# Kernel optimization log

Measured on AMD Instinct MI355X. Metric: run time of the kernel, lower is better.

The kernel has to match this reference:

```python
import jax, jax.numpy as jnp
import numpy as np

EPS = 1e-5
SLOPE = 0.2
K = 20
BINS = [1, 2, 4, 8, 16, 32]


def knn(x_t, k):
    # x_t: (B, N, C) -> idx (B, N, k) of nearest neighbors (by L2, incl. self)
    xx = jnp.sum(x_t * x_t, axis=-1)  # (B, N)
    pd = 2.0 * jnp.einsum('bnc,bmc->bnm', x_t, x_t) - xx[:, :, None] - xx[:, None, :]
    _, idx = jax.lax.top_k(pd, k)
    return idx


def edge_features(x_t, idx):
    # x_t: (B, N, C), idx: (B, N, k) -> (B, N, k, 2C) = [nbr - ctr, ctr]
    B = x_t.shape[0]
    nbr = x_t[jnp.arange(B)[:, None, None], idx]          # (B, N, k, C) gather
    ctr = jnp.broadcast_to(x_t[:, :, None, :], nbr.shape)
    return jnp.concatenate([nbr - ctr, ctr], axis=-1)


def batchnorm(h, gamma, beta, axes):
    # training-mode BN: normalize with batch statistics over `axes` (channel last)
    m = jnp.mean(h, axis=axes, keepdims=True)
    v = jnp.var(h, axis=axes, keepdims=True)
    return (h - m) * jax.lax.rsqrt(v + EPS) * gamma + beta


def lrelu(h):
    return jnp.where(h >= 0, h, SLOPE * h)


def edgeconv(x_t, W, g, b):
    # 1x1 conv over edge features + BN + LeakyReLU + max over k neighbors
    e = edge_features(x_t, knn(x_t, K))            # (B, N, k, 2C)
    h = jnp.einsum('bnkc,oc->bnko', e, W)          # per-edge GEMM
    h = lrelu(batchnorm(h, g, b, (0, 1, 2)))
    return jnp.max(h, axis=2)                      # (B, N, Cout)


def setup_inputs() -> dict:
    key = jax.random.key(0)
    ks = jax.random.split(key, 8)
    B, N = 4, 2048
    d = {'x': jax.random.normal(ks[0], (B, 3, N), dtype=jnp.float32)}
    # conv weights (out, in); BN gamma=1, beta=0 as in torch init
    d['W1'] = jax.random.normal(ks[1], (64, 6), dtype=jnp.float32) * 0.1
    d['g1'] = jnp.ones((64,), jnp.float32); d['b1'] = jnp.zeros((64,), jnp.float32)
    d['W2'] = jax.random.normal(ks[2], (64, 128), dtype=jnp.float32) * 0.1
    d['g2'] = jnp.ones((64,), jnp.float32); d['b2'] = jnp.zeros((64,), jnp.float32)
    d['W3'] = jax.random.normal(ks[3], (128, 128), dtype=jnp.float32) * 0.1
    d['g3'] = jnp.ones((128,), jnp.float32); d['b3'] = jnp.zeros((128,), jnp.float32)
    d['W4'] = jax.random.normal(ks[4], (256, 256), dtype=jnp.float32) * 0.1
    d['g4'] = jnp.ones((256,), jnp.float32); d['b4'] = jnp.zeros((256,), jnp.float32)
    d['W5'] = jax.random.normal(ks[5], (1024, 512), dtype=jnp.float32) * 0.05
    d['g5'] = jnp.ones((1024,), jnp.float32); d['b5'] = jnp.zeros((1024,), jnp.float32)
    d['Wf'] = jax.random.normal(ks[6], (256, 1024), dtype=jnp.float32) * 0.03
    d['bfeat'] = jax.random.normal(ks[7], (256,), dtype=jnp.float32) * 0.01
    return d


def reference(x, W1, g1, b1, W2, g2, b2, W3, g3, b3, W4, g4, b4, W5, g5, b5, Wf, bfeat):
    B, _, N = x.shape
    x_t = jnp.transpose(x, (0, 2, 1))              # (B, N, 3)
    x1 = edgeconv(x_t, W1, g1, b1)                 # (B, N, 64)
    x2 = edgeconv(x1, W2, g2, b2)                  # (B, N, 64)
    x3 = edgeconv(x2, W3, g3, b3)                  # (B, N, 128)
    x4 = edgeconv(x3, W4, g4, b4)                  # (B, N, 256)
    xc = jnp.concatenate([x1, x2, x3, x4], axis=-1)  # (B, N, 512)
    h = jnp.einsum('bnc,oc->bno', xc, W5)          # (B, N, 1024)
    h = lrelu(batchnorm(h, g5, b5, (0, 1)))
    F = h.shape[-1]
    feats = []
    for nb in BINS:  # horizontal pyramid pooling over contiguous point chunks
        z = h.reshape(B, nb, N // nb, F)
        feats.append(jnp.max(z, axis=2) + jnp.mean(z, axis=2))
    bins = jnp.concatenate(feats, axis=1)          # (B, 63, F)
    out = jnp.einsum('bsf,of->sbo', bins, Wf) + bfeat  # (63, B, 256)
    return out
```

## Files before the change

### kernel.cpp

```cpp
#include <hip/hip_runtime.h>
#include <hip/hip_bf16.h>
#include <cstdint>
#include <cstddef>

#define B_SZ   4
#define N_PTS  2048
#define KNN    20
#define BN_ROWS (B_SZ * N_PTS)
#define EPSV   1e-5f
#define SLOPEV 0.2f

typedef __attribute__((ext_vector_type(8))) short bf16x8;
typedef __attribute__((ext_vector_type(4))) float f32x4;

__global__ void k_transpose(const float* __restrict__ x, float* __restrict__ xt,
                            float* __restrict__ xx)
{
    int i = blockIdx.x * 256 + threadIdx.x;
    if (i >= BN_ROWS) return;
    int b = i >> 11, n = i & 2047;
    float v0 = x[((b * 3 + 0) << 11) + n];
    float v1 = x[((b * 3 + 1) << 11) + n];
    float v2 = x[((b * 3 + 2) << 11) + n];
    xt[i * 3 + 0] = v0; xt[i * 3 + 1] = v1; xt[i * 3 + 2] = v2;
    xx[i] = fmaf(v0, v0, fmaf(v1, v1, v2 * v2));
}

__global__ void k_prepw_all(const float* __restrict__ W1, const float* __restrict__ W2,
                            const float* __restrict__ W3, const float* __restrict__ W4,
                            const float* __restrict__ W5, const float* __restrict__ Wf,
                            float* __restrict__ wc, __hip_bfloat16* __restrict__ w5h,
                            float* __restrict__ wft)
{
    int i = blockIdx.x * 256 + threadIdx.x;
    if (i >= 876928) return;
    if (i >= 614784) {
        int e = i - 614784;
        int o = e >> 10, f = e & 1023;
        wft[f * 256 + o] = Wf[e];
        return;
    }
    if (i >= 90496) {
        int e = i - 90496;
        w5h[e] = __float2bfloat16(W5[e]);
        return;
    }
    const float* W; int O, C, off;
    if      (i < 384)   { W = W1; O = 64;  C = 3;   off = 0; }
    else if (i < 8576)  { W = W2; O = 64;  C = 64;  off = 384; }
    else if (i < 24960) { W = W3; O = 128; C = 64;  off = 8576; }
    else                { W = W4; O = 256; C = 128; off = 24960; }
    int e = i - off, j = e / C, c = e - j * C;
    float v;
    if (j < O) v = W[j * 2 * C + c];
    else { int jo = j - O; v = W[jo * 2 * C + C + c] - W[jo * 2 * C + c]; }
    wc[i] = v;
}

template<bool VEC>
__launch_bounds__(512)
__global__ void k_dist(const float* __restrict__ A, int lda,
                       const float* __restrict__ xx,
                       float* __restrict__ C1, int Kd)
{
    constexpr int LDA_ = 132;
    constexpr int LDT_ = 68;
    __shared__ float smem[8704];
    float* As = smem;
    float* Bs = smem + 32 * LDA_;
    float* T  = smem;
    const int tid = threadIdx.x;
    const int tx  = tid & 31;
    const int ty  = tid >> 5;

    int t = blockIdx.x;
    int it, jt;
    if (t < 120) {
        int i = 0;
        for (; i < 15; ++i) { int cnt = 15 - i; if (t < cnt) break; t -= cnt; }
        it = i; jt = i + 1 + t;
    } else {
        it = jt = t - 120;
    }
    const int m0 = it * 128;
    const int n0 = jt * 128;
    const int b  = blockIdx.z;
    const float* Ab = A + (size_t)b * N_PTS * lda;

    float acc[2][4][4] = {};

    for (int k0 = 0; k0 < Kd; k0 += 32) {
        #pragma unroll
        for (int r = 0; r < 2; ++r) {
            int e = r * 512 + tid, row = e >> 3, kq = e & 7;
            if constexpr (VEC) {
                float4 v = *(const float4*)&Ab[(size_t)(m0 + row) * lda + k0 + kq * 4];
                As[(kq * 4 + 0) * LDA_ + row] = v.x;
                As[(kq * 4 + 1) * LDA_ + row] = v.y;
                As[(kq * 4 + 2) * LDA_ + row] = v.z;
                As[(kq * 4 + 3) * LDA_ + row] = v.w;
            } else {
                #pragma unroll
                for (int j = 0; j < 4; ++j) {
                    int kg = k0 + kq * 4 + j;
                    As[(kq * 4 + j) * LDA_ + row] =
                        (kg < Kd) ? Ab[(size_t)(m0 + row) * lda + kg] : 0.f;
                }
            }
        }
        #pragma unroll
        for (int r = 0; r < 2; ++r) {
            int e = r * 512 + tid, row = e >> 3, kq = e & 7;
            if constexpr (VEC) {
                float4 v = *(const float4*)&Ab[(size_t)(n0 + row) * lda + k0 + kq * 4];
                Bs[(kq * 4 + 0) * LDA_ + row] = v.x;
                Bs[(kq * 4 + 1) * LDA_ + row] = v.y;
                Bs[(kq * 4 + 2) * LDA_ + row] = v.z;
                Bs[(kq * 4 + 3) * LDA_ + row] = v.w;
            } else {
                #pragma unroll
                for (int j = 0; j < 4; ++j) {
                    int kg = k0 + kq * 4 + j;
                    Bs[(kq * 4 + j) * LDA_ + row] =
                        (kg < Kd) ? Ab[(size_t)(n0 + row) * lda + kg] : 0.f;
                }
            }
        }
        __syncthreads();

        if constexpr (VEC) {
            float4 ca0 = *(const float4*)&As[ty * 4];
            float4 ca1 = *(const float4*)&As[64 + ty * 4];
            float4 cb  = *(const float4*)&Bs[tx * 4];
            #pragma unroll
            for (int kk = 0; kk < 32; ++kk) {
                float4 na0, na1, nb;
                if (kk < 31) {
                    na0 = *(const float4*)&As[(kk + 1) * LDA_ + ty * 4];
                    na1 = *(const float4*)&As[(kk + 1) * LDA_ + 64 + ty * 4];
                    nb  = *(const float4*)&Bs[(kk + 1) * LDA_ + tx * 4];
                }
                float av[2][4] = {{ca0.x,ca0.y,ca0.z,ca0.w},{ca1.x,ca1.y,ca1.z,ca1.w}};
                float bw[4] = {cb.x, cb.y, cb.z, cb.w};
                #pragma unroll
                for (int ih = 0; ih < 2; ++ih)
                    #pragma unroll
                    for (int ii = 0; ii < 4; ++ii)
                        #pragma unroll
                        for (int jj = 0; jj < 4; ++jj)
                            acc[ih][ii][jj] = fmaf(av[ih][ii], bw[jj], acc[ih][ii][jj]);
                if (kk < 31) { ca0 = na0; ca1 = na1; cb = nb; }
            }
        } else {
            int klen = Kd - k0; if (klen > 32) klen = 32;
            #pragma unroll 8
            for (int kk = 0; kk < klen; ++kk) {
                float4 a0 = *(const float4*)&As[kk * LDA_ + ty * 4];
                float4 a1 = *(const float4*)&As[kk * LDA_ + 64 + ty * 4];
                float4 bq = *(const float4*)&Bs[kk * LDA_ + tx * 4];
                float av[2][4] = {{a0.x,a0.y,a0.z,a0.w},{a1.x,a1.y,a1.z,a1.w}};
                float bw[4] = {bq.x, bq.y, bq.z, bq.w};
                #pragma unroll
                for (int ih = 0; ih < 2; ++ih)
                    #pragma unroll
                    for (int ii = 0; ii < 4; ++ii)
                        #pragma unroll
                        for (int jj = 0; jj < 4; ++jj)
                            acc[ih][ii][jj] = fmaf(av[ih][ii], bw[jj], acc[ih][ii][jj]);
            }
        }
        __syncthreads();
    }

    const float* xxb = xx + b * N_PTS;
    float xj[4];
    {
        float4 v = *(const float4*)&xxb[n0 + tx * 4];
        xj[0] = v.x; xj[1] = v.y; xj[2] = v.z; xj[3] = v.w;
    }
    float xiv[2][4];
    #pragma unroll
    for (int ih = 0; ih < 2; ++ih)
        #pragma unroll
        for (int i = 0; i < 4; ++i)
            xiv[ih][i] = xxb[m0 + ih * 64 + ty * 4 + i];
    const bool diag = (m0 == n0);
    const size_t zoff = (size_t)b * N_PTS;

    #pragma unroll
    for (int ih = 0; ih < 2; ++ih)
        #pragma unroll
        for (int i = 0; i < 4; ++i) {
            int gi = m0 + ih * 64 + ty * 4 + i;
            float xi = xiv[ih][i];
            int gj = n0 + tx * 4;
            float4 v;
            v.x = 2.f * acc[ih][i][0] - xi - xj[0];
            v.y = 2.f * acc[ih][i][1] - xi - xj[1];
            v.z = 2.f * acc[ih][i][2] - xi - xj[2];
            v.w = 2.f * acc[ih][i][3] - xi - xj[3];
            if (diag) {
                if (gi == gj + 0) v.x = 0.f;
                if (gi == gj + 1) v.y = 0.f;
                if (gi == gj + 2) v.z = 0.f;
                if (gi == gj + 3) v.w = 0.f;
            }
            *(float4*)&C1[(zoff + gi) * N_PTS + gj] = v;
        }

    if (!diag) {
        #pragma unroll
        for (int ih = 0; ih < 2; ++ih) {
            #pragma unroll
            for (int c = 0; c < 4; ++c) {
                float xjc = xj[c];
                float4 tv;
                tv.x = 2.f * acc[ih][0][c] - xjc - xiv[ih][0];
                tv.y = 2.f * acc[ih][1][c] - xjc - xiv[ih][1];
                tv.z = 2.f * acc[ih][2][c] - xjc - xiv[ih][2];
                tv.w = 2.f * acc[ih][3][c] - xjc - xiv[ih][3];
                *(float4*)&T[(tx * 4 + c) * LDT_ + ty * 4] = tv;
            }
            __syncthreads();
            #pragma unroll
            for (int r = 0; r < 4; ++r) {
                int e = r * 512 + tid;
                int jr = e >> 4, c4 = e & 15;
                float4 tv = *(const float4*)&T[jr * LDT_ + c4 * 4];
                *(float4*)&C1[(zoff + n0 + jr) * N_PTS + m0 + ih * 64 + c4 * 4] = tv;
            }
            __syncthreads();
        }
    }
}

__launch_bounds__(256)
__global__ void k_gemm5(const unsigned short* __restrict__ Ah,
                        const unsigned short* __restrict__ Bh,
                        float* __restrict__ Cf,
                        float* __restrict__ ssum, float* __restrict__ ssumsq)
{
    constexpr int LDA = 72;
    __shared__ unsigned short As[128 * LDA];
    __shared__ unsigned short Bs[128 * LDA];
    const int tid  = threadIdx.x;
    const int lane = tid & 63;
    const int w    = tid >> 6;
    const int wr   = w >> 1, wcl = w & 1;
    const int quad = lane >> 4;
    const int l16  = lane & 15;
    const int m0 = blockIdx.y * 128;
    const int n0 = blockIdx.x * 128;

    f32x4 acc[4][4] = {};

    for (int k0 = 0; k0 < 512; k0 += 64) {
        #pragma unroll
        for (int r = 0; r < 4; ++r) {
            int e = r * 256 + tid, row = e >> 3, kq = e & 7;
            *(uint4*)&As[row * LDA + kq * 8] =
                *(const uint4*)&Ah[(size_t)(m0 + row) * 512 + k0 + kq * 8];
        }
        #pragma unroll
        for (int r = 0; r < 4; ++r) {
            int e = r * 256 + tid, row = e >> 3, kq = e & 7;
            *(uint4*)&Bs[row * LDA + kq * 8] =
                *(const uint4*)&Bh[(size_t)(n0 + row) * 512 + k0 + kq * 8];
        }
        __syncthreads();
        #pragma unroll
        for (int kk = 0; kk < 64; kk += 32) {
            bf16x8 af[4], bfr[4];
            #pragma unroll
            for (int i = 0; i < 4; ++i)
                af[i] = *(const bf16x8*)&As[(wr * 64 + i * 16 + l16) * LDA + kk + quad * 8];
            #pragma unroll
            for (int j = 0; j < 4; ++j)
                bfr[j] = *(const bf16x8*)&Bs[(wcl * 64 + j * 16 + l16) * LDA + kk + quad * 8];
            #pragma unroll
            for (int i = 0; i < 4; ++i)
                #pragma unroll
                for (int j = 0; j < 4; ++j)
                    acc[i][j] = __builtin_amdgcn_mfma_f32_16x16x32_bf16(af[i], bfr[j], acc[i][j], 0, 0, 0);
        }
        __syncthreads();
    }

    #pragma unroll
    for (int i = 0; i < 4; ++i) {
        int rbase = m0 + wr * 64 + i * 16 + quad * 4;
        #pragma unroll
        for (int j = 0; j < 4; ++j) {
            int col = n0 + wcl * 64 + j * 16 + l16;
            #pragma unroll
            for (int r = 0; r < 4; ++r)
                Cf[(size_t)(rbase + r) * 1024 + col] = acc[i][j][r];
        }
    }

    float* sredS = (float*)As;
    float* sredQ = (float*)Bs;
    #pragma unroll
    for (int j = 0; j < 4; ++j) {
        float s = 0.f, q = 0.f;
        #pragma unroll
        for (int i = 0; i < 4; ++i)
            #pragma unroll
            for (int r = 0; r < 4; ++r) {
                float v = acc[i][j][r];
                s += v; q = fmaf(v, v, q);
            }
        int coll = wcl * 64 + j * 16 + l16;
        int slot = wr * 4 + quad;
        sredS[coll * 8 + slot] = s;
        sredQ[coll * 8 + slot] = q;
    }
    __syncthreads();
    if (tid < 128) {
        float s = 0.f, q = 0.f;
        #pragma unroll
        for (int t = 0; t < 8; ++t) { s += sredS[tid * 8 + t]; q += sredQ[tid * 8 + t]; }
        ssum  [blockIdx.y * 1024 + n0 + tid] = s;
        ssumsq[blockIdx.y * 1024 + n0 + tid] = q;
    }
}

template<bool VEC>
__launch_bounds__(256)
__global__ void k_selgd(const float* __restrict__ D2, int* __restrict__ idx_out,
                        const float* __restrict__ A, int lda,
                        const float* __restrict__ Bm, int ldb,
                        float* __restrict__ C1, float* __restrict__ C2,
                        int Nn, int Kd, int gdBlocks, int gdsh)
{
    constexpr int LDA_ = 132;
    constexpr int LDB_ = 68;
    __shared__ float smem[32 * LDA_ + 32 * LDB_];

    if ((int)blockIdx.x < gdBlocks) {
        float* As = smem;
        float* Bs = smem + 32 * LDA_;
        const int tid = threadIdx.x;
        const int tx  = tid & 15;
        const int ty  = tid >> 4;
        const int gdx = Nn >> 6;
        const int bx  = blockIdx.x & (gdx - 1);
        const int by  = blockIdx.x >> gdsh;
        const int m0 = by * 128;
        const int n0 = bx * 64;

        float acc[2][4][4] = {};

        for (int k0 = 0; k0 < Kd; k0 += 32) {
            #pragma unroll
            for (int r = 0; r < 4; ++r) {
                int e = r * 256 + tid, row = e >> 3, kq = e & 7;
                if constexpr (VEC) {
                    float4 v = *(const float4*)&A[(size_t)(m0 + row) * lda + k0 + kq * 4];
                    As[(kq * 4 + 0) * LDA_ + row] = v.x;
                    As[(kq * 4 + 1) * LDA_ + row] = v.y;
                    As[(kq * 4 + 2) * LDA_ + row] = v.z;
                    As[(kq * 4 + 3) * LDA_ + row] = v.w;
                } else {
                    #pragma unroll
                    for (int j = 0; j < 4; ++j) {
                        int kg = k0 + kq * 4 + j;
                        As[(kq * 4 + j) * LDA_ + row] =
                            (kg < Kd) ? A[(size_t)(m0 + row) * lda + kg] : 0.f;
                    }
                }
            }
            #pragma unroll
            for (int r = 0; r < 2; ++r) {
                int e = r * 256 + tid, row = e >> 3, kq = e & 7;
                if constexpr (VEC) {
                    float4 v = *(const float4*)&Bm[(size_t)(n0 + row) * ldb + k0 + kq * 4];
                    Bs[(kq * 4 + 0) * LDB_ + row] = v.x;
                    Bs[(kq * 4 + 1) * LDB_ + row] = v.y;
                    Bs[(kq * 4 + 2) * LDB_ + row] = v.z;
                    Bs[(kq * 4 + 3) * LDB_ + row] = v.w;
                } else {
                    #pragma unroll
                    for (int j = 0; j < 4; ++j) {
                        int kg = k0 + kq * 4 + j;
                        Bs[(kq * 4 + j) * LDB_ + row] =
                            (kg < Kd) ? Bm[(size_t)(n0 + row) * ldb + kg] : 0.f;
                    }
                }
            }
            __syncthreads();

            if constexpr (VEC) {
                float4 ca0 = *(const float4*)&As[ty * 4];
                float4 ca1 = *(const float4*)&As[64 + ty * 4];
                float4 cb0 = *(const float4*)&Bs[tx * 4];
                #pragma unroll
                for (int kk = 0; kk < 32; ++kk) {
                    float4 na0, na1, nb0;
                    if (kk < 31) {
                        na0 = *(const float4*)&As[(kk + 1) * LDA_ + ty * 4];
                        na1 = *(const float4*)&As[(kk + 1) * LDA_ + 64 + ty * 4];
                        nb0 = *(const float4*)&Bs[(kk + 1) * LDB_ + tx * 4];
                    }
                    float av[2][4] = {{ca0.x,ca0.y,ca0.z,ca0.w},{ca1.x,ca1.y,ca1.z,ca1.w}};
                    float bw[4] = {cb0.x, cb0.y, cb0.z, cb0.w};
                    #pragma unroll
                    for (int ih = 0; ih < 2; ++ih)
                        #pragma unroll
                        for (int ii = 0; ii < 4; ++ii)
                            #pragma unroll
                            for (int jj = 0; jj < 4; ++jj)
                                acc[ih][ii][jj] = fmaf(av[ih][ii], bw[jj], acc[ih][ii][jj]);
                    if (kk < 31) { ca0 = na0; ca1 = na1; cb0 = nb0; }
                }
            } else {
                int klen = Kd - k0; if (klen > 32) klen = 32;
                #pragma unroll 8
                for (int kk = 0; kk < klen; ++kk) {
                    float4 a0 = *(const float4*)&As[kk * LDA_ + ty * 4];
                    float4 a1 = *(const float4*)&As[kk * LDA_ + 64 + ty * 4];
                    float4 bq = *(const float4*)&Bs[kk * LDB_ + tx * 4];
                    float av[2][4] = {{a0.x,a0.y,a0.z,a0.w},{a1.x,a1.y,a1.z,a1.w}};
                    float bw[4] = {bq.x, bq.y, bq.z, bq.w};
                    #pragma unroll
                    for (int ih = 0; ih < 2; ++ih)
                        #pragma unroll
                        for (int ii = 0; ii < 4; ++ii)
                            #pragma unroll
                            for (int jj = 0; jj < 4; ++jj)
                                acc[ih][ii][jj] = fmaf(av[ih][ii], bw[jj], acc[ih][ii][jj]);
                }
            }
            __syncthreads();
        }

        const int Oo = Nn >> 1;
        #pragma unroll
        for (int ih = 0; ih < 2; ++ih)
            #pragma unroll
            for (int i = 0; i < 4; ++i) {
                int row = m0 + ih * 64 + ty * 4 + i;
                int colg = n0 + tx * 4;
                float4 v = make_float4(acc[ih][i][0], acc[ih][i][1],
                                       acc[ih][i][2], acc[ih][i][3]);
                if (colg < Oo) *(float4*)&C1[(size_t)row * Oo + colg] = v;
                else           *(float4*)&C2[(size_t)row * Oo + colg - Oo] = v;
            }
        return;
    }

    const int lane = threadIdx.x & 63;
    const int w    = threadIdx.x >> 6;
    const int qloc = ((int)blockIdx.x - gdBlocks) * 4 + w;
    const float* row = D2 + (size_t)qloc * N_PTS;

    unsigned key[32];
    #pragma unroll
    for (int c = 0; c < 8; ++c) {
        float4 v = *(const float4*)&row[c * 256 + lane * 4];
        float vv[4] = {v.x, v.y, v.z, v.w};
        #pragma unroll
        for (int r = 0; r < 4; ++r) {
            unsigned u = __float_as_uint(vv[r]);
            key[c * 4 + r] = ((int)u >= 0) ? (u | 0x80000000u) : ~u;
        }
    }

    unsigned lmax = 0u;
    #pragma unroll
    for (int e = 0; e < 32; ++e) lmax = (key[e] > lmax) ? key[e] : lmax;
    unsigned gmin = lmax, gmax = lmax;
    #pragma unroll
    for (int s = 32; s >= 1; s >>= 1) {
        unsigned o1 = __shfl_xor(gmin, s, 64);
        unsigned o2 = __shfl_xor(gmax, s, 64);
        gmin = (o1 < gmin) ? o1 : gmin;
        gmax = (o2 > gmax) ? o2 : gmax;
    }
    unsigned lo = gmin, hi = gmax;

    while (hi - lo >= 65536u) {
        unsigned mid = lo + ((hi - lo) >> 1);
        int cnt = 0;
        #pragma unroll
        for (int e = 0; e < 32; ++e)
            cnt += __popcll(__ballot(key[e] > mid));
        if (cnt < KNN) hi = mid; else lo = mid + 1;
    }

    if (lo < hi) {
        int cAbove = 0;
        #pragma unroll
        for (int e = 0; e < 32; ++e)
            cAbove += __popcll(__ballot(key[e] > hi));
        unsigned c0 = 0u, c1 = 0u, c2 = 0u, c3 = 0u;
        int nc = 0;
        #pragma unroll
        for (int e = 0; e < 32; ++e) {
            unsigned k = key[e];
            if (k >= lo && k <= hi) {
                if (nc == 0) c0 = k; else if (nc == 1) c1 = k;
                else if (nc == 2) c2 = k; else if (nc == 3) c3 = k;
                ++nc;
            }
        }
        if (__ballot(nc > 4)) {
            while (lo < hi) {
                unsigned mid = lo + ((hi - lo) >> 1);
                int cnt = 0;
                #pragma unroll
                for (int e = 0; e < 32; ++e)
                    cnt += __popcll(__ballot(key[e] > mid));
                if (cnt < KNN) hi = mid; else lo = mid + 1;
            }
        } else {
            while (lo < hi) {
                unsigned mid = lo + ((hi - lo) >> 1);
                int cnt = cAbove
                        + __popcll(__ballot(c0 > mid))
                        + __popcll(__ballot(c1 > mid))
                        + __popcll(__ballot(c2 > mid))
                        + __popcll(__ballot(c3 > mid));
                if (cnt < KNN) hi = mid; else lo = mid + 1;
            }
        }
    }
    const unsigned T = lo;

    int* outp = idx_out + (size_t)qloc * KNN;
    const unsigned long long ltmask = (lane == 0) ? 0ull : (~0ull >> (64 - lane));
    int base = 0;
    #pragma unroll
    for (int e = 0; e < 32; ++e) {
        bool p = key[e] > T;
        unsigned long long m = __ballot(p);
        if (p) {
            int pos = base + __popcll(m & ltmask);
            outp[pos] = (e >> 2) * 256 + lane * 4 + (e & 3);
        }
        base += __popcll(m);
    }
    #pragma unroll
    for (int e = 0; e < 32; ++e) {
        bool p = key[e] == T;
        unsigned long long m = __ballot(p);
        if (p) {
            int pos = base + __popcll(m & ltmask);
            if (pos < KNN) outp[pos] = (e >> 2) * 256 + lane * 4 + (e & 3);
        }
        base += __popcll(m);
    }
}

template<int O, int NSEQ>
__launch_bounds__(256)
__global__ void k_gather(const float* __restrict__ gtab, const float* __restrict__ dtab,
                         const int* __restrict__ idx,
                         float* __restrict__ hmax, float* __restrict__ hmin,
                         float* __restrict__ ssum, float* __restrict__ ssumsq)
{
    constexpr int NPB = 256 / O;
    const int grp = threadIdx.x / O;
    const int o   = threadIdx.x & (O - 1);
    float accS = 0.f, accS2 = 0.f;
    const int rowsPerBlock = NPB * NSEQ;
    const int batch = blockIdx.x & 3;
    const int chunk = blockIdx.x >> 2;
    const int bbase = batch << 11;
    for (int s = 0; s < NSEQ; ++s) {
        int row = bbase + chunk * rowsPerBlock + s * NPB + grp;
        const int* ip = idx + (size_t)row * KNN;
        float gmax = -INFINITY, gmin = INFINITY, gs = 0.f, gs2 = 0.f;
        for (int k = 0; k < KNN; ++k) {
            int nb = ip[k];
            float v = gtab[(size_t)(bbase + nb) * O + o];
            gmax = fmaxf(gmax, v);
            gmin = fminf(gmin, v);
            gs  += v;
            gs2  = fmaf(v, v, gs2);
        }
        float d = dtab[(size_t)row * O + o];
        hmax[(size_t)row * O + o] = gmax + d;
        hmin[(size_t)row * O + o] = gmin + d;
        accS  += gs + (float)KNN * d;
        accS2 += gs2 + 2.f * d * gs + (float)KNN * d * d;
    }
    int bank = blockIdx.x & 63;
    atomicAdd(&ssum[bank * O + o], accS);
    atomicAdd(&ssumsq[bank * O + o], accS2);
}

template<int O, bool WRITE_XX>
__launch_bounds__(256)
__global__ void k_normalize(const float* __restrict__ hmax, const float* __restrict__ hmin,
                            const float* __restrict__ ssum, const float* __restrict__ ssumsq,
                            const float* __restrict__ gamma, const float* __restrict__ beta,
                            float invM, float* __restrict__ xcs,
                            __hip_bfloat16* __restrict__ xch, float* __restrict__ xx)
{
    const int tid = threadIdx.x;
    const int o   = tid & (O - 1);
    float s = 0.f, s2 = 0.f;
    #pragma unroll 8
    for (int bk = 0; bk < 64; ++bk) { s += ssum[bk * O + o]; s2 += ssumsq[bk * O + o]; }
    float mean = s * invM;
    float var  = fmaf(-mean, mean, s2 * invM);
    float sc   = gamma[o] * rsqrtf(var + EPSV);
    float sh   = beta[o] - mean * sc;

    constexpr int R = 256 / O;
    const int rloc = tid / O;
    __shared__ float part[4];
    const int ngroups = BN_ROWS / R;
    for (int gidx = blockIdx.x; gidx < ngroups; gidx += gridDim.x) {
        int row = gidx * R + rloc;
        size_t i = (size_t)row * O + o;
        float h = (sc >= 0.f) ? hmax[i] : hmin[i];
        float y = fmaf(h, sc, sh);
        y = (y >= 0.f) ? y : SLOPEV * y;
        xcs[(size_t)row * 512 + o] = y;
        xch[(size_t)row * 512 + o] = __float2bfloat16(y);
        if constexpr (WRITE_XX) {
            float p = y * y;
            #pragma unroll
            for (int sft = 32; sft >= 1; sft >>= 1) p += __shfl_xor(p, sft, 64);
            if constexpr (O == 64) {
                if ((tid & 63) == 0) xx[row] = p;
            } else {
                if ((tid & 63) == 0) part[tid >> 6] = p;
                __syncthreads();
                if constexpr (O == 128) {
                    if (tid < 2) xx[gidx * R + tid] = part[2 * tid] + part[2 * tid + 1];
                } else {
                    if (tid == 0) xx[gidx * R] = (part[0] + part[1]) + (part[2] + part[3]);
                }
                __syncthreads();
            }
        }
    }
}

__global__ void k_seg(const float* __restrict__ h,
                      const float* __restrict__ ssum, const float* __restrict__ ssumsq,
                      const float* __restrict__ gamma, const float* __restrict__ beta,
                      float* __restrict__ smax, float* __restrict__ ssumseg)
{
    int f = blockIdx.y * 256 + threadIdx.x;
    float s = 0.f, s2 = 0.f;
    #pragma unroll 8
    for (int bk = 0; bk < 64; ++bk) { s += ssum[bk * 1024 + f]; s2 += ssumsq[bk * 1024 + f]; }
    const float invM = 1.f / (float)BN_ROWS;
    float mean = s * invM;
    float var  = fmaf(-mean, mean, s2 * invM);
    float sc   = gamma[f] * rsqrtf(var + EPSV);
    float sh   = beta[f] - mean * sc;

    int seg = blockIdx.x;
    float mx = -INFINITY, sm = 0.f;
    int n0 = seg * 64;
    for (int i = 0; i < 64; ++i) {
        float v = fmaf(h[(size_t)(n0 + i) * 1024 + f], sc, sh);
        v = (v >= 0.f) ? v : SLOPEV * v;
        mx = fmaxf(mx, v); sm += v;
    }
    smax[(size_t)seg * 1024 + f]    = mx;
    ssumseg[(size_t)seg * 1024 + f] = sm;
}

__launch_bounds__(256)
__global__ void k_final(const float* __restrict__ smax, const float* __restrict__ ssg,
                        const float* __restrict__ Wft, const float* __restrict__ bfeat,
                        float* __restrict__ out)
{
    __shared__ float row[1024];
    __shared__ float part[1024];
    const int tid = threadIdx.x;
    int sb = blockIdx.x;
    int s = sb >> 2, b = sb & 3;
    int nb = (s == 0) ? 1 : (s < 3) ? 2 : (s < 7) ? 4 : (s < 15) ? 8 : (s < 31) ? 16 : 32;
    int idxL = s - (nb - 1);
    int segc = 32 / nb;
    int seg0 = b * 32 + idxL * segc;
    float inv = 1.f / (float)(64 * segc);
    for (int c = tid; c < 1024; c += 256) {
        float mx = -INFINITY, sm = 0.f;
        for (int t = 0; t < segc; ++t) {
            mx = fmaxf(mx, smax[(size_t)(seg0 + t) * 1024 + c]);
            sm += ssg[(size_t)(seg0 + t) * 1024 + c];
        }
        row[c] = mx + sm * inv;
    }
    __syncthreads();

    const int lane = tid & 63;
    const int w    = tid >> 6;
    const float* rw = row + w * 256;
    const float* wp = Wft + (size_t)(w * 256) * 256 + lane * 4;
    float4 a0 = {0,0,0,0}, a1 = {0,0,0,0}, a2 = {0,0,0,0}, a3 = {0,0,0,0};
    for (int f = 0; f < 256; f += 4) {
        float r0 = rw[f + 0], r1 = rw[f + 1], r2 = rw[f + 2], r3 = rw[f + 3];
        float4 w0 = *(const float4*)&wp[(size_t)(f + 0) * 256];
        float4 w1 = *(const float4*)&wp[(size_t)(f + 1) * 256];
        float4 w2 = *(const float4*)&wp[(size_t)(f + 2) * 256];
        float4 w3 = *(const float4*)&wp[(size_t)(f + 3) * 256];
        a0.x = fmaf(r0, w0.x, a0.x); a0.y = fmaf(r0, w0.y, a0.y);
        a0.z = fmaf(r0, w0.z, a0.z); a0.w = fmaf(r0, w0.w, a0.w);
        a1.x = fmaf(r1, w1.x, a1.x); a1.y = fmaf(r1, w1.y, a1.y);
        a1.z = fmaf(r1, w1.z, a1.z); a1.w = fmaf(r1, w1.w, a1.w);
        a2.x = fmaf(r2, w2.x, a2.x); a2.y = fmaf(r2, w2.y, a2.y);
        a2.z = fmaf(r2, w2.z, a2.z); a2.w = fmaf(r2, w2.w, a2.w);
        a3.x = fmaf(r3, w3.x, a3.x); a3.y = fmaf(r3, w3.y, a3.y);
        a3.z = fmaf(r3, w3.z, a3.z); a3.w = fmaf(r3, w3.w, a3.w);
    }
    float4 a;
    a.x = (a0.x + a1.x) + (a2.x + a3.x);
    a.y = (a0.y + a1.y) + (a2.y + a3.y);
    a.z = (a0.z + a1.z) + (a2.z + a3.z);
    a.w = (a0.w + a1.w) + (a2.w + a3.w);
    *(float4*)&part[w * 256 + lane * 4] = a;
    __syncthreads();
    int o = tid;
    float acc = (part[o] + part[256 + o]) + (part[512 + o] + part[768 + o]);
    out[(size_t)sb * 256 + o] = acc + bfeat[o];
}

extern "C" void kernel_launch(void* const* d_in, const int* in_sizes, int n_in,
                              void* d_out, int out_size, void* d_ws, size_t ws_size,
                              hipStream_t stream)
{
    const float* x  = (const float*)d_in[0];
    const float* W1 = (const float*)d_in[1];
    const float* g1 = (const float*)d_in[2];
    const float* b1 = (const float*)d_in[3];
    const float* W2 = (const float*)d_in[4];
    const float* g2 = (const float*)d_in[5];
    const float* b2 = (const float*)d_in[6];
    const float* W3 = (const float*)d_in[7];
    const float* g3 = (const float*)d_in[8];
    const float* b3 = (const float*)d_in[9];
    const float* W4 = (const float*)d_in[10];
    const float* g4 = (const float*)d_in[11];
    const float* b4 = (const float*)d_in[12];
    const float* W5 = (const float*)d_in[13];
    const float* g5 = (const float*)d_in[14];
    const float* b5 = (const float*)d_in[15];
    const float* Wf = (const float*)d_in[16];
    const float* bfeat = (const float*)d_in[17];
    float* out = (float*)d_out;
    float* ws  = (float*)d_ws;

    float* xt1   = ws + 0;
    int*   idx   = (int*)(ws + 24576);
    float* xx    = ws + 188416;
    float* xc    = ws + 196608;
    float* hmax  = ws + 4390912;
    float* hmin  = ws + 6488064;
    float* stats = ws + 8585216;
    float* smax  = ws + 8650752;
    float* ssg   = ws + 8781824;
    float* wc    = ws + 8912896;
    float* big   = ws + 9003520;
    __hip_bfloat16* xch = (__hip_bfloat16*)(ws + 25780736);
    __hip_bfloat16* w5h = (__hip_bfloat16*)(ws + 27877888);
    float* wft   = ws + 28140032;
    float* l5s   = ws + 28402176;
    float* l5q   = ws + 28467712;
    float* gtab  = ws + 28533248;
    float* dtab  = ws + 30630400;

    hipMemsetAsync(stats, 0, 65536 * sizeof(float), stream);
    k_transpose<<<32, 256, 0, stream>>>(x, xt1, xx);
    k_prepw_all<<<3426, 256, 0, stream>>>(W1, W2, W3, W4, W5, Wf, wc, w5h, wft);

    const float invMk = 1.f / (float)(BN_ROWS * KNN);

    {
        float* ss = stats + 0;
        k_dist<false><<<dim3(136, 1, 4), 512, 0, stream>>>(xt1, 3, xx, big, 3);
        k_selgd<false><<<128 + 2048, 256, 0, stream>>>(big, idx, xt1, 3, wc, 3, gtab, dtab, 128, 3, 128, 1);
        k_gather<64, 8><<<256, 256, 0, stream>>>(gtab, dtab, idx, hmax, hmin, ss, ss + 4096);
        k_normalize<64, true><<<512, 256, 0, stream>>>(hmax, hmin, ss, ss + 4096, g1, b1, invMk, xc + 0, xch + 0, xx);
    }
    {
        float* ss = stats + 8192;
        k_dist<true><<<dim3(136, 1, 4), 512, 0, stream>>>(xc + 0, 512, xx, big, 64);
        k_selgd<true><<<128 + 2048, 256, 0, stream>>>(big, idx, xc + 0, 512, wc + 384, 64, gtab, dtab, 128, 64, 128, 1);
        k_gather<64, 8><<<256, 256, 0, stream>>>(gtab, dtab, idx, hmax, hmin, ss, ss + 4096);
        k_normalize<64, true><<<512, 256, 0, stream>>>(hmax, hmin, ss, ss + 4096, g2, b2, invMk, xc + 64, xch + 64, xx);
    }
    {
        float* ss = stats + 16384;
        k_dist<true><<<dim3(136, 1, 4), 512, 0, stream>>>(xc + 64, 512, xx, big, 64);
        k_selgd<true><<<256 + 2048, 256, 0, stream>>>(big, idx, xc + 64, 512, wc + 8576, 64, gtab, dtab, 256, 64, 256, 2);
        k_gather<128, 8><<<512, 256, 0, stream>>>(gtab, dtab, idx, hmax, hmin, ss, ss + 8192);
        k_normalize<128, true><<<512, 256, 0, stream>>>(hmax, hmin, ss, ss + 8192, g3, b3, invMk, xc + 128, xch + 128, xx);
    }
    {
        float* ss = stats + 32768;
        k_dist<true><<<dim3(136, 1, 4), 512, 0, stream>>>(xc + 128, 512, xx, big, 128);
        k_selgd<true><<<512 + 2048, 256, 0, stream>>>(big, idx, xc + 128, 512, wc + 24960, 128, gtab, dtab, 512, 128, 512, 3);
        k_gather<256, 8><<<1024, 256, 0, stream>>>(gtab, dtab, idx, hmax, hmin, ss, ss + 16384);
        k_normalize<256, false><<<512, 256, 0, stream>>>(hmax, hmin, ss, ss + 16384, g4, b4, invMk, xc + 256, xch + 256, xx);
    }
    {
        k_gemm5<<<dim3(8, 64), 256, 0, stream>>>((const unsigned short*)xch, (const unsigned short*)w5h, big, l5s, l5q);
        k_seg<<<dim3(128, 4), 256, 0, stream>>>(big, l5s, l5q, g5, b5, smax, ssg);
        k_final<<<252, 256, 0, stream>>>(smax, ssg, wft, bfeat, out);
    }
}
```

Before: 490.3 us.

## Pre-select max/min by gamma sign in gather and rework top-k threshold search

The gather kernel now writes a single buffer holding either the per-channel max or min, chosen by the sign of gamma (since sc = gamma*rsqrt(var+eps) has gamma's sign). This halves the gather kernel's writes and the normalize kernel's reads. The selection kernel's threshold search now first binary-searches on per-lane maxima, then collects candidates at or above that bound, falling back to a full-key search if any lane has more than four. This is meant to cut ballot iterations, but it may cost extra iterations when many lanes overflow.

Result: no change. 488.2 us (median of 3 runs) (-0.4%).

```diff
diff --git a/kernel.cpp b/kernel.cpp
--- a/kernel.cpp
+++ b/kernel.cpp
@@ -477,52 +477,43 @@
         gmin = (o1 < gmin) ? o1 : gmin;
         gmax = (o2 > gmax) ? o2 : gmax;
     }
-    unsigned lo = gmin, hi = gmax;
-
-    while (hi - lo >= 65536u) {
-        unsigned mid = lo + ((hi - lo) >> 1);
-        int cnt = 0;
-        #pragma unroll
-        for (int e = 0; e < 32; ++e)
-            cnt += __popcll(__ballot(key[e] > mid));
-        if (cnt < KNN) hi = mid; else lo = mid + 1;
-    }
-
-    if (lo < hi) {
-        int cAbove = 0;
-        #pragma unroll
-        for (int e = 0; e < 32; ++e)
-            cAbove += __popcll(__ballot(key[e] > hi));
-        unsigned c0 = 0u, c1 = 0u, c2 = 0u, c3 = 0u;
-        int nc = 0;
-        #pragma unroll
-        for (int e = 0; e < 32; ++e) {
-            unsigned k = key[e];
-            if (k >= lo && k <= hi) {
-                if (nc == 0) c0 = k; else if (nc == 1) c1 = k;
-                else if (nc == 2) c2 = k; else if (nc == 3) c3 = k;
-                ++nc;
-            }
-        }
-        if (__ballot(nc > 4)) {
-            while (lo < hi) {
-                unsigned mid = lo + ((hi - lo) >> 1);
-                int cnt = 0;
-                #pragma unroll
-                for (int e = 0; e < 32; ++e)
-                    cnt += __popcll(__ballot(key[e] > mid));
-                if (cnt < KNN) hi = mid; else lo = mid + 1;
-            }
-        } else {
-            while (lo < hi) {
-                unsigned mid = lo + ((hi - lo) >> 1);
-                int cnt = cAbove
-                        + __popcll(__ballot(c0 > mid))
-                        + __popcll(__ballot(c1 > mid))
-                        + __popcll(__ballot(c2 > mid))
-                        + __popcll(__ballot(c3 > mid));
-                if (cnt < KNN) hi = mid; else lo = mid + 1;
-            }
+
+    unsigned lo = gmin, hi2 = gmax;
+    while (lo < hi2) {
+        unsigned mid = lo + ((hi2 - lo) >> 1);
+        int c = __popcll(__ballot(lmax > mid));
+        if (c < KNN) hi2 = mid; else lo = mid + 1;
+    }
+    unsigned hi = gmax;
+
+    unsigned c0 = 0u, c1 = 0u, c2 = 0u, c3 = 0u;
+    int nc = 0;
+    #pragma unroll
+    for (int e = 0; e < 32; ++e) {
+        unsigned k = key[e];
+        if (k >= lo) {
+            if (nc == 0) c0 = k; else if (nc == 1) c1 = k;
+            else if (nc == 2) c2 = k; else if (nc == 3) c3 = k;
+            ++nc;
+        }
+    }
+    if (__ballot(nc > 4)) {
+        while (lo < hi) {
+            unsigned mid = lo + ((hi - lo) >> 1);
+            int cnt = 0;
+            #pragma unroll
+            for (int e = 0; e < 32; ++e)
+                cnt += __popcll(__ballot(key[e] > mid));
+            if (cnt < KNN) hi = mid; else lo = mid + 1;
+        }
+    } else {
+        while (lo < hi) {
+            unsigned mid = lo + ((hi - lo) >> 1);
+            int cnt = __popcll(__ballot(c0 > mid))
+                    + __popcll(__ballot(c1 > mid))
+                    + __popcll(__ballot(c2 > mid))
+                    + __popcll(__ballot(c3 > mid));
+            if (cnt < KNN) hi = mid; else lo = mid + 1;
         }
     }
     const unsigned T = lo;
@@ -555,13 +546,14 @@
 template<int O, int NSEQ>
 __launch_bounds__(256)
 __global__ void k_gather(const float* __restrict__ gtab, const float* __restrict__ dtab,
-                         const int* __restrict__ idx,
-                         float* __restrict__ hmax, float* __restrict__ hmin,
+                         const int* __restrict__ idx, const float* __restrict__ gamma,
+                         float* __restrict__ hsel,
                          float* __restrict__ ssum, float* __restrict__ ssumsq)
 {
     constexpr int NPB = 256 / O;
     const int grp = threadIdx.x / O;
     const int o   = threadIdx.x & (O - 1);
+    const float g = gamma[o];
     float accS = 0.f, accS2 = 0.f;
     const int rowsPerBlock = NPB * NSEQ;
     const int batch = blockIdx.x & 3;
@@ -580,8 +572,8 @@
             gs2  = fmaf(v, v, gs2);
         }
         float d = dtab[(size_t)row * O + o];
-        hmax[(size_t)row * O + o] = gmax + d;
-        hmin[(size_t)row * O + o] = gmin + d;
+        float keep = (g >= 0.f) ? gmax : gmin;
+        hsel[(size_t)row * O + o] = keep + d;
         accS  += gs + (float)KNN * d;
         accS2 += gs2 + 2.f * d * gs + (float)KNN * d * d;
     }
@@ -592,7 +584,7 @@
 
 template<int O, bool WRITE_XX>
 __launch_bounds__(256)
-__global__ void k_normalize(const float* __restrict__ hmax, const float* __restrict__ hmin,
+__global__ void k_normalize(const float* __restrict__ hsel,
                             const float* __restrict__ ssum, const float* __restrict__ ssumsq,
                             const float* __restrict__ gamma, const float* __restrict__ beta,
                             float invM, float* __restrict__ xcs,
@@ -615,7 +607,7 @@
     for (int gidx = blockIdx.x; gidx < ngroups; gidx += gridDim.x) {
         int row = gidx * R + rloc;
         size_t i = (size_t)row * O + o;
-        float h = (sc >= 0.f) ? hmax[i] : hmin[i];
+        float h = hsel[i];
         float y = fmaf(h, sc, sh);
         y = (y >= 0.f) ? y : SLOPEV * y;
         xcs[(size_t)row * 512 + o] = y;
@@ -753,8 +745,7 @@
     int*   idx   = (int*)(ws + 24576);
     float* xx    = ws + 188416;
     float* xc    = ws + 196608;
-    float* hmax  = ws + 4390912;
-    float* hmin  = ws + 6488064;
+    float* hsel  = ws + 4390912;
     float* stats = ws + 8585216;
     float* smax  = ws + 8650752;
     float* ssg   = ws + 8781824;
@@ -778,29 +769,29 @@
         float* ss = stats + 0;
         k_dist<false><<<dim3(136, 1, 4), 512, 0, stream>>>(xt1, 3, xx, big, 3);
         k_selgd<false><<<128 + 2048, 256, 0, stream>>>(big, idx, xt1, 3, wc, 3, gtab, dtab, 128, 3, 128, 1);
-        k_gather<64, 8><<<256, 256, 0, stream>>>(gtab, dtab, idx, hmax, hmin, ss, ss + 4096);
-        k_normalize<64, true><<<512, 256, 0, stream>>>(hmax, hmin, ss, ss + 4096, g1, b1, invMk, xc + 0, xch + 0, xx);
+        k_gather<64, 8><<<256, 256, 0, stream>>>(gtab, dtab, idx, g1, hsel, ss, ss + 4096);
+        k_normalize<64, true><<<512, 256, 0, stream>>>(hsel, ss, ss + 4096, g1, b1, invMk, xc + 0, xch + 0, xx);
     }
     {
         float* ss = stats + 8192;
         k_dist<true><<<dim3(136, 1, 4), 512, 0, stream>>>(xc + 0, 512, xx, big, 64);
         k_selgd<true><<<128 + 2048, 256, 0, stream>>>(big, idx, xc + 0, 512, wc + 384, 64, gtab, dtab, 128, 64, 128, 1);
-        k_gather<64, 8><<<256, 256, 0, stream>>>(gtab, dtab, idx, hmax, hmin, ss, ss + 4096);
-        k_normalize<64, true><<<512, 256, 0, stream>>>(hmax, hmin, ss, ss + 4096, g2, b2, invMk, xc + 64, xch + 64, xx);
+        k_gather<64, 8><<<256, 256, 0, stream>>>(gtab, dtab, idx, g2, hsel, ss, ss + 4096);
+        k_normalize<64, true><<<512, 256, 0, stream>>>(hsel, ss, ss + 4096, g2, b2, invMk, xc + 64, xch + 64, xx);
     }
     {
         float* ss = stats + 16384;
         k_dist<true><<<dim3(136, 1, 4), 512, 0, stream>>>(xc + 64, 512, xx, big, 64);
         k_selgd<true><<<256 + 2048, 256, 0, stream>>>(big, idx, xc + 64, 512, wc + 8576, 64, gtab, dtab, 256, 64, 256, 2);
-        k_gather<128, 8><<<512, 256, 0, stream>>>(gtab, dtab, idx, hmax, hmin, ss, ss + 8192);
-        k_normalize<128, true><<<512, 256, 0, stream>>>(hmax, hmin, ss, ss + 8192, g3, b3, invMk, xc + 128, xch + 128, xx);
+        k_gather<128, 8><<<512, 256, 0, stream>>>(gtab, dtab, idx, g3, hsel, ss, ss + 8192);
+        k_normalize<128, true><<<512, 256, 0, stream>>>(hsel, ss, ss + 8192, g3, b3, invMk, xc + 128, xch + 128, xx);
     }
     {
         float* ss = stats + 32768;
         k_dist<true><<<dim3(136, 1, 4), 512, 0, stream>>>(xc + 128, 512, xx, big, 128);
         k_selgd<true><<<512 + 2048, 256, 0, stream>>>(big, idx, xc + 128, 512, wc + 24960, 128, gtab, dtab, 512, 128, 512, 3);
-        k_gather<256, 8><<<1024, 256, 0, stream>>>(gtab, dtab, idx, hmax, hmin, ss, ss + 16384);
-        k_normalize<256, false><<<512, 256, 0, stream>>>(hmax, hmin, ss, ss + 16384, g4, b4, invMk, xc + 256, xch + 256, xx);
+        k_gather<256, 8><<<1024, 256, 0, stream>>>(gtab, dtab, idx, g4, hsel, ss, ss + 16384);
+        k_normalize<256, false><<<512, 256, 0, stream>>>(hsel, ss, ss + 16384, g4, b4, invMk, xc + 256, xch + 256, xx);
     }
     {
         k_gemm5<<<dim3(8, 64), 256, 0, stream>>>((const unsigned short*)xch, (const unsigned short*)w5h, big, l5s, l5q);
```
